# Kernel tuning notes

Hardware: AMD Instinct MI355X
Metric: run time of the kernel (lower is better)

## Reference

```python
import jax, jax.numpy as jnp
import numpy as np

N_NODES = 100000


def setup_inputs() -> dict:
    key = jax.random.key(0)
    ks = jax.random.split(key, 9)
    x = jax.random.normal(ks[0], (N_NODES, 500), dtype=jnp.float32)
    # lin1: Linear(m=500, hidden=64, bias=False) -> weight [hidden, m]
    W1 = jax.random.normal(ks[1], (64, 500), dtype=jnp.float32) * 0.02
    # lin_final: Linear(3*hidden=192, m_y=10, bias=False) -> weight [m_y, 3*hidden]
    Wf = jax.random.normal(ks[2], (10, 192), dtype=jnp.float32) * 0.02
    # 1-hop normalized adjacency in COO form (600k nnz)
    src1 = jax.random.randint(ks[3], (600000,), 0, N_NODES, dtype=jnp.int32)
    dst1 = jax.random.randint(ks[4], (600000,), 0, N_NODES, dtype=jnp.int32)
    val1 = jax.random.uniform(ks[5], (600000,), dtype=jnp.float32)
    # 2-hop normalized adjacency in COO form (1.2M nnz)
    src2 = jax.random.randint(ks[6], (1200000,), 0, N_NODES, dtype=jnp.int32)
    dst2 = jax.random.randint(ks[7], (1200000,), 0, N_NODES, dtype=jnp.int32)
    val2 = jax.random.uniform(ks[8], (1200000,), dtype=jnp.float32)
    return {"x": x, "W1": W1, "Wf": Wf,
            "src1": src1, "dst1": dst1, "val1": val1,
            "src2": src2, "dst2": dst2, "val2": val2}


def _spmm(src, dst, val, h):
    # sparse.mm(A, h): out[dst] += val * h[src]
    return jax.ops.segment_sum(val[:, None] * h[src], dst, num_segments=N_NODES)


def reference(x, W1, Wf, src1, dst1, val1, src2, dst2, val2):
    h = jax.nn.relu(x @ W1.T)                 # [N, hidden]
    h1 = _spmm(src1, dst1, val1, h)           # [N, hidden]
    h2 = _spmm(src2, dst2, val2, h)           # [N, hidden]
    h_final = jnp.concatenate([h, h1, h2], axis=1)  # [N, 3*hidden]
    # dropout is identity in eval mode
    return h_final @ Wf.T                     # [N, m_y]
```

## Files before the change

### kernel.cpp

```cpp
#include <hip/hip_runtime.h>
#include <hip/hip_bf16.h>

#define NN   100000
#define KD   500
#define HID  64
#define LWS  264

typedef short frag8 __attribute__((ext_vector_type(8)));
typedef float f32x4 __attribute__((ext_vector_type(4)));

static __device__ __forceinline__ unsigned short f2b(float f) {
    return __builtin_bit_cast(unsigned short, __float2bfloat16(f));
}

__global__ __launch_bounds__(256, 4) void k1_mfma(const float* __restrict__ x,
                                                  const float* __restrict__ W1,
                                                  float* __restrict__ h, int n)
{
    __shared__ unsigned short lw[64 * LWS];
    const int tid   = threadIdx.x;
    const int lane  = tid & 63;
    const int wid   = tid >> 6;
    const int l15   = lane & 15;
    const int l4    = lane >> 4;
    const int koffl = 8 * l4;

    const long rowBlk = (long)blockIdx.x * 128 + wid * 32;
    long ra0 = rowBlk + l15;       if (ra0 >= n) ra0 = n - 1;
    long ra1 = rowBlk + 16 + l15;  if (ra1 >= n) ra1 = n - 1;
    const float* xp0 = x + ra0 * KD + koffl;
    const float* xp1 = x + ra1 * KD + koffl;

    f32x4 acc[2][4] = {};

    for (int c = 0; c < 2; ++c) {
        if (c) __syncthreads();
        for (int it = 0; it < 16; ++it) {
            const int idx = tid + it * 256;
            const int r   = idx >> 6;
            const int q   = idx & 63;
            const int kg  = c * 256 + 4 * q;
            float4 v = make_float4(0.f, 0.f, 0.f, 0.f);
            if (kg < KD) v = *(const float4*)&W1[(long)r * KD + kg];
            ushort4 pk;
            pk.x = f2b(v.x); pk.y = f2b(v.y); pk.z = f2b(v.z); pk.w = f2b(v.w);
            *(ushort4*)&lw[r * LWS + 4 * q] = pk;
        }
        __syncthreads();

        #pragma unroll 2
        for (int ks = 0; ks < 8; ++ks) {
            const int k0 = c * 256 + ks * 32;
            const int kb = k0 + koffl;
            const float4 z = make_float4(0.f, 0.f, 0.f, 0.f);
            const float4 lo0 = (kb     < KD) ? *(const float4*)(xp0 + k0)     : z;
            const float4 hi0 = (kb + 4 < KD) ? *(const float4*)(xp0 + k0 + 4) : z;
            const float4 lo1 = (kb     < KD) ? *(const float4*)(xp1 + k0)     : z;
            const float4 hi1 = (kb + 4 < KD) ? *(const float4*)(xp1 + k0 + 4) : z;
            frag8 a0, a1;
            a0[0]=f2b(lo0.x); a0[1]=f2b(lo0.y); a0[2]=f2b(lo0.z); a0[3]=f2b(lo0.w);
            a0[4]=f2b(hi0.x); a0[5]=f2b(hi0.y); a0[6]=f2b(hi0.z); a0[7]=f2b(hi0.w);
            a1[0]=f2b(lo1.x); a1[1]=f2b(lo1.y); a1[2]=f2b(lo1.z); a1[3]=f2b(lo1.w);
            a1[4]=f2b(hi1.x); a1[5]=f2b(hi1.y); a1[6]=f2b(hi1.z); a1[7]=f2b(hi1.w);
            const int koffw = ks * 32 + koffl;
            #pragma unroll
            for (int g = 0; g < 4; ++g) {
                const frag8 b = *(const frag8*)&lw[(g * 16 + l15) * LWS + koffw];
                acc[0][g] = __builtin_amdgcn_mfma_f32_16x16x32_bf16(a0, b, acc[0][g], 0, 0, 0);
                acc[1][g] = __builtin_amdgcn_mfma_f32_16x16x32_bf16(a1, b, acc[1][g], 0, 0, 0);
            }
        }
    }

    #pragma unroll
    for (int rb = 0; rb < 2; ++rb) {
        #pragma unroll
        for (int r = 0; r < 4; ++r) {
            const long row = rowBlk + rb * 16 + l4 * 4 + r;
            if (row < n) {
                #pragma unroll
                for (int g = 0; g < 4; ++g)
                    h[row * HID + g * 16 + l15] = fmaxf(acc[rb][g][r], 0.f);
            }
        }
    }
}

__global__ __launch_bounds__(256) void k2_proj(const float* __restrict__ h,
                                               const float* __restrict__ Wf,
                                               float* __restrict__ out,
                                               float* __restrict__ g, int n)
{
    __shared__ float lwf[10 * 196];
    const int tid = threadIdx.x;
    for (int idx = tid; idx < 480; idx += 256) {
        const int j = idx / 48;
        const int q = idx - j * 48;
        const float4 v = *(const float4*)&Wf[j * 192 + 4 * q];
        *(float4*)&lwf[j * 196 + 4 * q] = v;
    }
    __syncthreads();

    const long row = (long)blockIdx.x * 8 + (tid >> 5);
    const int  j   = tid & 31;
    if (row < n && j < 30) {
        const int wrow = (j < 10) ? j : ((j < 20) ? j - 10 : j - 20);
        const int coff = (j < 10) ? 0 : ((j < 20) ? 64 : 128);
        const float* wp = &lwf[wrow * 196 + coff];
        const float* hp = &h[row * HID];
        float s = 0.f;
        #pragma unroll
        for (int q = 0; q < 16; ++q) {
            const float4 hv = *(const float4*)&hp[4 * q];
            const float4 wv = *(const float4*)&wp[4 * q];
            s += hv.x * wv.x + hv.y * wv.y + hv.z * wv.z + hv.w * wv.w;
        }
        if (j < 10) out[row * 10 + j] = s;
        else        g[row * 20 + (j - 10)] = s;
    }
}

__global__ __launch_bounds__(256) void k_scatter(const int* __restrict__ src,
                                                 const int* __restrict__ dst,
                                                 const float* __restrict__ val,
                                                 const float* __restrict__ g,
                                                 float* __restrict__ out,
                                                 int nnz, int goff)
{
    const int t = blockIdx.x * 256 + threadIdx.x;
    if (t >= nnz * 10) return;
    const int e = t / 10;
    const int j = t - e * 10;
    const int s = src[e];
    const int d = dst[e];
    const float v = val[e];
    unsafeAtomicAdd(&out[(size_t)d * 10 + j], v * g[(size_t)s * 20 + goff + j]);
}

extern "C" void kernel_launch(void* const* d_in, const int* in_sizes, int n_in,
                              void* d_out, int out_size, void* d_ws, size_t ws_size,
                              hipStream_t stream)
{
    const float* x    = (const float*)d_in[0];
    const float* W1   = (const float*)d_in[1];
    const float* Wf   = (const float*)d_in[2];
    const int*   src1 = (const int*)d_in[3];
    const int*   dst1 = (const int*)d_in[4];
    const float* val1 = (const float*)d_in[5];
    const int*   src2 = (const int*)d_in[6];
    const int*   dst2 = (const int*)d_in[7];
    const float* val2 = (const float*)d_in[8];
    const int nnz1 = in_sizes[3];
    const int nnz2 = in_sizes[6];
    const int n = NN;

    float* h = (float*)d_ws;
    float* g = h + (size_t)NN * HID;
    float* out = (float*)d_out;

    k1_mfma<<<(n + 127) / 128, 256, 0, stream>>>(x, W1, h, n);
    k2_proj<<<(n + 7) / 8, 256, 0, stream>>>(h, Wf, out, g, n);
    k_scatter<<<(nnz1 * 10 + 255) / 256, 256, 0, stream>>>(src1, dst1, val1, g, out, nnz1, 0);
    k_scatter<<<(nnz2 * 10 + 255) / 256, 256, 0, stream>>>(src2, dst2, val2, g, out, nnz2, 10);
}
```

Before: 257.1 us.

## Pre-convert W1 to bf16, shrink GEMM tiles, merge scatter launches per-edge

Adds a small kernel that converts W1 to padded bf16 once per call, so each GEMM block copies bf16 into LDS instead of converting it. Tiles drop to 64 rows per block, one 16-row tile per wave, and the x loads are software-prefetched one step ahead. The two scatter launches become one kernel with a thread per edge instead of per edge-column, so src/dst/val are read once per edge. g is padded to stride 24 to allow vector loads. The trade-off is more GEMM blocks and an extra launch, in exchange for higher occupancy and less repeated index traffic.

```diff
diff --git a/kernel.cpp b/kernel.cpp
--- a/kernel.cpp
+++ b/kernel.cpp
@@ -3,8 +3,10 @@
 
 #define NN   100000
 #define KD   500
+#define KP   512
 #define HID  64
 #define LWS  264
+#define GS   24
 
 typedef short frag8 __attribute__((ext_vector_type(8)));
 typedef float f32x4 __attribute__((ext_vector_type(4)));
@@ -13,8 +15,18 @@
     return __builtin_bit_cast(unsigned short, __float2bfloat16(f));
 }
 
+__global__ __launch_bounds__(256) void k0_w1bf(const float* __restrict__ W1,
+                                               unsigned short* __restrict__ W1bf)
+{
+    const int i = blockIdx.x * 256 + threadIdx.x;
+    const int c = i >> 9;
+    const int k = i & 511;
+    const float v = (k < KD) ? W1[c * KD + k] : 0.f;
+    W1bf[i] = f2b(v);
+}
+
 __global__ __launch_bounds__(256, 4) void k1_mfma(const float* __restrict__ x,
-                                                  const float* __restrict__ W1,
+                                                  const unsigned short* __restrict__ W1bf,
                                                   float* __restrict__ h, int n)
 {
     __shared__ unsigned short lw[64 * LWS];
@@ -25,63 +37,58 @@
     const int l4    = lane >> 4;
     const int koffl = 8 * l4;
 
-    const long rowBlk = (long)blockIdx.x * 128 + wid * 32;
-    long ra0 = rowBlk + l15;       if (ra0 >= n) ra0 = n - 1;
-    long ra1 = rowBlk + 16 + l15;  if (ra1 >= n) ra1 = n - 1;
-    const float* xp0 = x + ra0 * KD + koffl;
-    const float* xp1 = x + ra1 * KD + koffl;
+    const long rowBlk = (long)blockIdx.x * 64;
+    long ra = rowBlk + wid * 16 + l15;
+    if (ra >= n) ra = n - 1;
+    const float* xp = x + ra * KD + koffl;
 
-    f32x4 acc[2][4] = {};
+    f32x4 acc[4] = {};
+    const float4 z = make_float4(0.f, 0.f, 0.f, 0.f);
 
     for (int c = 0; c < 2; ++c) {
         if (c) __syncthreads();
-        for (int it = 0; it < 16; ++it) {
+        #pragma unroll
+        for (int it = 0; it < 8; ++it) {
             const int idx = tid + it * 256;
-            const int r   = idx >> 6;
-            const int q   = idx & 63;
-            const int kg  = c * 256 + 4 * q;
-            float4 v = make_float4(0.f, 0.f, 0.f, 0.f);
-            if (kg < KD) v = *(const float4*)&W1[(long)r * KD + kg];
-            ushort4 pk;
-            pk.x = f2b(v.x); pk.y = f2b(v.y); pk.z = f2b(v.z); pk.w = f2b(v.w);
-            *(ushort4*)&lw[r * LWS + 4 * q] = pk;
+            const int r   = idx >> 5;
+            const int q   = idx & 31;
+            *(uint4*)&lw[r * LWS + q * 8] =
+                *(const uint4*)&W1bf[r * KP + c * 256 + q * 8];
         }
         __syncthreads();
 
-        #pragma unroll 2
+        int k0 = c * 256;
+        float4 lo = (k0 + koffl     < KD) ? *(const float4*)(xp + k0)     : z;
+        float4 hi = (k0 + koffl + 4 < KD) ? *(const float4*)(xp + k0 + 4) : z;
+
+        #pragma unroll
         for (int ks = 0; ks < 8; ++ks) {
-            const int k0 = c * 256 + ks * 32;
-            const int kb = k0 + koffl;
-            const float4 z = make_float4(0.f, 0.f, 0.f, 0.f);
-            const float4 lo0 = (kb     < KD) ? *(const float4*)(xp0 + k0)     : z;
-            const float4 hi0 = (kb + 4 < KD) ? *(const float4*)(xp0 + k0 + 4) : z;
-            const float4 lo1 = (kb     < KD) ? *(const float4*)(xp1 + k0)     : z;
-            const float4 hi1 = (kb + 4 < KD) ? *(const float4*)(xp1 + k0 + 4) : z;
-            frag8 a0, a1;
-            a0[0]=f2b(lo0.x); a0[1]=f2b(lo0.y); a0[2]=f2b(lo0.z); a0[3]=f2b(lo0.w);
-            a0[4]=f2b(hi0.x); a0[5]=f2b(hi0.y); a0[6]=f2b(hi0.z); a0[7]=f2b(hi0.w);
-            a1[0]=f2b(lo1.x); a1[1]=f2b(lo1.y); a1[2]=f2b(lo1.z); a1[3]=f2b(lo1.w);
-            a1[4]=f2b(hi1.x); a1[5]=f2b(hi1.y); a1[6]=f2b(hi1.z); a1[7]=f2b(hi1.w);
+            float4 nlo = z, nhi = z;
+            if (ks < 7) {
+                const int kn = c * 256 + (ks + 1) * 32;
+                nlo = (kn + koffl     < KD) ? *(const float4*)(xp + kn)     : z;
+                nhi = (kn + koffl + 4 < KD) ? *(const float4*)(xp + kn + 4) : z;
+            }
+            frag8 a;
+            a[0]=f2b(lo.x); a[1]=f2b(lo.y); a[2]=f2b(lo.z); a[3]=f2b(lo.w);
+            a[4]=f2b(hi.x); a[5]=f2b(hi.y); a[6]=f2b(hi.z); a[7]=f2b(hi.w);
             const int koffw = ks * 32 + koffl;
             #pragma unroll
             for (int g = 0; g < 4; ++g) {
                 const frag8 b = *(const frag8*)&lw[(g * 16 + l15) * LWS + koffw];
-                acc[0][g] = __builtin_amdgcn_mfma_f32_16x16x32_bf16(a0, b, acc[0][g], 0, 0, 0);
-                acc[1][g] = __builtin_amdgcn_mfma_f32_16x16x32_bf16(a1, b, acc[1][g], 0, 0, 0);
+                acc[g] = __builtin_amdgcn_mfma_f32_16x16x32_bf16(a, b, acc[g], 0, 0, 0);
             }
+            lo = nlo; hi = nhi;
         }
     }
 
     #pragma unroll
-    for (int rb = 0; rb < 2; ++rb) {
-        #pragma unroll
-        for (int r = 0; r < 4; ++r) {
-            const long row = rowBlk + rb * 16 + l4 * 4 + r;
-            if (row < n) {
-                #pragma unroll
-                for (int g = 0; g < 4; ++g)
-                    h[row * HID + g * 16 + l15] = fmaxf(acc[rb][g][r], 0.f);
-            }
+    for (int r = 0; r < 4; ++r) {
+        const long row = rowBlk + wid * 16 + l4 * 4 + r;
+        if (row < n) {
+            #pragma unroll
+            for (int g = 0; g < 4; ++g)
+                h[row * HID + g * 16 + l15] = fmaxf(acc[g][r], 0.f);
         }
     }
 }
@@ -115,26 +122,47 @@
             const float4 wv = *(const float4*)&wp[4 * q];
             s += hv.x * wv.x + hv.y * wv.y + hv.z * wv.z + hv.w * wv.w;
         }
-        if (j < 10) out[row * 10 + j] = s;
-        else        g[row * 20 + (j - 10)] = s;
+        if (j < 10)      out[row * 10 + j] = s;
+        else if (j < 20) g[row * GS + (j - 10)] = s;
+        else             g[row * GS + 12 + (j - 20)] = s;
     }
 }
 
-__global__ __launch_bounds__(256) void k_scatter(const int* __restrict__ src,
-                                                 const int* __restrict__ dst,
-                                                 const float* __restrict__ val,
+__global__ __launch_bounds__(256) void k_scatter(const int* __restrict__ src1,
+                                                 const int* __restrict__ dst1,
+                                                 const float* __restrict__ val1, int nnz1,
+                                                 const int* __restrict__ src2,
+                                                 const int* __restrict__ dst2,
+                                                 const float* __restrict__ val2, int nnz2,
                                                  const float* __restrict__ g,
-                                                 float* __restrict__ out,
-                                                 int nnz, int goff)
+                                                 float* __restrict__ out)
 {
-    const int t = blockIdx.x * 256 + threadIdx.x;
-    if (t >= nnz * 10) return;
-    const int e = t / 10;
-    const int j = t - e * 10;
-    const int s = src[e];
-    const int d = dst[e];
-    const float v = val[e];
-    unsafeAtomicAdd(&out[(size_t)d * 10 + j], v * g[(size_t)s * 20 + goff + j]);
+    const int e = blockIdx.x * 256 + threadIdx.x;
+    const int* sp; const int* dp; const float* vp; int goff, idx;
+    if (e < nnz1) { sp = src1; dp = dst1; vp = val1; goff = 0;  idx = e; }
+    else {
+        idx = e - nnz1;
+        if (idx >= nnz2) return;
+        sp = src2; dp = dst2; vp = val2; goff = 12;
+    }
+    const int   s = sp[idx];
+    const int   d = dp[idx];
+    const float v = vp[idx];
+    const float* gp = g + (size_t)s * GS + goff;
+    const float4 g0 = *(const float4*)gp;
+    const float4 g1 = *(const float4*)(gp + 4);
+    const float2 g2 = *(const float2*)(gp + 8);
+    float* op = out + (size_t)d * 10;
+    unsafeAtomicAdd(op + 0, v * g0.x);
+    unsafeAtomicAdd(op + 1, v * g0.y);
+    unsafeAtomicAdd(op + 2, v * g0.z);
+    unsafeAtomicAdd(op + 3, v * g0.w);
+    unsafeAtomicAdd(op + 4, v * g1.x);
+    unsafeAtomicAdd(op + 5, v * g1.y);
+    unsafeAtomicAdd(op + 6, v * g1.z);
+    unsafeAtomicAdd(op + 7, v * g1.w);
+    unsafeAtomicAdd(op + 8, v * g2.x);
+    unsafeAtomicAdd(op + 9, v * g2.y);
 }
 
 extern "C" void kernel_launch(void* const* d_in, const int* in_sizes, int n_in,
@@ -154,12 +182,15 @@
     const int nnz2 = in_sizes[6];
     const int n = NN;
 
-    float* h = (float*)d_ws;
-    float* g = h + (size_t)NN * HID;
+    unsigned short* W1bf = (unsigned short*)d_ws;
+    float* h   = (float*)((char*)d_ws + 64 * KP * 2);
+    float* g   = h + (size_t)NN * HID;
     float* out = (float*)d_out;
 
-    k1_mfma<<<(n + 127) / 128, 256, 0, stream>>>(x, W1, h, n);
+    k0_w1bf<<<128, 256, 0, stream>>>(W1, W1bf);
+    k1_mfma<<<(n + 63) / 64, 256, 0, stream>>>(x, W1bf, h, n);
     k2_proj<<<(n + 7) / 8, 256, 0, stream>>>(h, Wf, out, g, n);
-    k_scatter<<<(nnz1 * 10 + 255) / 256, 256, 0, stream>>>(src1, dst1, val1, g, out, nnz1, 0);
-    k_scatter<<<(nnz2 * 10 + 255) / 256, 256, 0, stream>>>(src2, dst2, val2, g, out, nnz2, 10);
+    const int ne = nnz1 + nnz2;
+    k_scatter<<<(ne + 255) / 256, 256, 0, stream>>>(src1, dst1, val1, nnz1,
+                                                    src2, dst2, val2, nnz2, g, out);
 }
```

Measured after the change: 996.7 us. 288% more time.
